# Optimization experiments

Hardware: AMD Instinct MI355X
Metric: run time of the kernel (lower is better)

## Reference

```python
import jax, jax.numpy as jnp
import numpy as np

B, N, C, H, W = 4, 8, 256, 64, 64
SCALE = 2
D = C * SCALE  # embed_dim*scale, head_size with n_heads=1
EPS = 1e-6


def setup_inputs() -> dict:
    key = jax.random.key(0)
    ks = jax.random.split(key, 6)
    sc = lambda k, sh, f: jax.random.normal(k, sh, jnp.float32) * f
    return {
        "q": jax.random.normal(ks[0], (B, C), jnp.float32),
        "c": jax.random.normal(ks[1], (B, N, C, H, W), jnp.float32),
        "g": jnp.ones((C,), jnp.float32),                 # RMSNorm weight
        "Wq": sc(ks[2], (D, C), C ** -0.5),               # proj_q weight
        "Wkv": sc(ks[3], (2 * D, C), C ** -0.5),          # proj_kv weight
        "Wo": sc(ks[4], (C, D), D ** -0.5),               # proj_out weight
        "bo": jnp.zeros((C,), jnp.float32),               # proj_out bias
    }


def reference(q, c, g, Wq, Wkv, Wo, bo):
    # c: [B,N,C,H,W] -> [B,H,W,N,C]
    cp = jnp.transpose(c, (0, 3, 4, 1, 2))
    # RMSNorm over channel dim
    cn = cp * jax.lax.rsqrt(jnp.mean(cp * cp, axis=-1, keepdims=True) + EPS) * g
    # per-pixel, per-token k/v projection: [B,H,W,N,2D]
    kv = jnp.einsum('bhwnc,dc->bhwnd', cn, Wkv)
    k, v = jnp.split(kv, 2, axis=-1)                      # each [B,H,W,N,D]
    qp = q @ Wq.T                                         # [B,D]
    # broadcast single query over spatial grid; softmax over N context tokens
    dots = jnp.einsum('bd,bhwnd->bhwn', qp, k) * (D ** -0.5)
    att = jax.nn.softmax(dots, axis=-1)                   # [B,H,W,N]
    hvec = jnp.einsum('bhwn,bhwnd->bhwd', att, v)         # [B,H,W,D]
    out = hvec @ Wo.T + bo                                # [B,H,W,C]
    return jnp.transpose(out, (0, 3, 1, 2))               # [B,C,H,W]
```

## Files before the change

### kernel.cpp

```cpp
#include <hip/hip_runtime.h>


typedef __attribute__((ext_vector_type(8))) short short8;
typedef __attribute__((ext_vector_type(4))) float floatx4;

static __device__ __forceinline__ short f2bf(float f) {
  unsigned u = __float_as_uint(f);
  u += 0x7fffu + ((u >> 16) & 1u);
  return (short)(u >> 16);
}

__global__ __launch_bounds__(256) void pre_kernel(
    const float* __restrict__ q, const float* __restrict__ g,
    const float* __restrict__ Wq, const float* __restrict__ Wkv,
    const float* __restrict__ Wo, unsigned char* __restrict__ ws) {
  short* WovgB = (short*)ws;
  float* gqk = (float*)(ws + 131072);
  const int blk = blockIdx.x, tid = threadIdx.x;
  if (blk < 256) {
    const int i = blk, c = tid;
    float s = 0.f;
    #pragma unroll 16
    for (int d = 0; d < 512; ++d)
      s = fmaf(Wo[i * 512 + d], Wkv[(512 + d) * 256 + c], s);
    const int it = i >> 4, m = i & 15;
    const int sg = c >> 5, q2 = (c >> 3) & 3, jj = c & 7;
    WovgB[((((it * 8 + sg) * 4 + q2) * 16) + m) * 8 + jj] = f2bf(s * g[c]);
  } else {
    const int b = blk - 256;
    __shared__ float qps[512];
    for (int d = tid; d < 512; d += 256) {
      float s = 0.f;
      #pragma unroll 16
      for (int cc = 0; cc < 256; ++cc)
        s = fmaf(Wq[d * 256 + cc], q[b * 256 + cc], s);
      qps[d] = s;
    }
    __syncthreads();
    const int c = tid;
    float s = 0.f;
    #pragma unroll 16
    for (int d = 0; d < 512; ++d)
      s = fmaf(Wkv[d * 256 + c], qps[d], s);
    gqk[b * 256 + c] = s * g[c] * 0.044194173824159216f;
  }
}

__global__ __launch_bounds__(256, 2) void attn_kernel(
    const float* __restrict__ cin, const float* __restrict__ bo,
    const unsigned char* __restrict__ ws, float* __restrict__ out) {
  const short8* Av = (const short8*)ws;
  const float* gqk = (const float*)(ws + 131072);
  const int blk = blockIdx.x;
  const int b = blk >> 7, h = (blk >> 1) & 63, hf = blk & 1;
  const int tid = threadIdx.x;
  const int lane = tid & 63, w = tid >> 6;
  const int px = lane & 31, cgh = lane >> 5;
  const int cg = w * 2 + cgh;

  __shared__ short tB[8][2][64][8];
  __shared__ float redS[2][4][32], redD[2][4][32];

  float rg[32];
  #pragma unroll
  for (int j = 0; j < 32; ++j) rg[j] = gqk[b * 256 + cg * 32 + j];

  float t_reg[32];
  #pragma unroll
  for (int j = 0; j < 32; ++j) t_reg[j] = 0.f;
  float mM = -1e30f, zZ = 0.f;

  const float* cb = cin + ((size_t)(b * 8) * 256 + cg * 32) * 4096
                        + h * 64 + hf * 32 + px;
  for (int n = 0; n < 8; ++n) {
    const float* cp = cb + (size_t)n * 256 * 4096;
    float vals[32];
    #pragma unroll
    for (int j = 0; j < 32; ++j) vals[j] = cp[(size_t)j * 4096];
    float ssq = 0.f, dt = 0.f;
    #pragma unroll
    for (int j = 0; j < 32; ++j) {
      ssq = fmaf(vals[j], vals[j], ssq);
      dt = fmaf(vals[j], rg[j], dt);
    }
    ssq += __shfl_xor(ssq, 32);
    dt  += __shfl_xor(dt, 32);
    if (cgh == 0) { redS[n & 1][w][px] = ssq; redD[n & 1][w][px] = dt; }
    __syncthreads();
    float S = 0.f, Dt = 0.f;
    #pragma unroll
    for (int ww = 0; ww < 4; ++ww) { S += redS[n & 1][ww][px]; Dt += redD[n & 1][ww][px]; }
    const float invr = rsqrtf(S * (1.f / 256.f) + 1e-6f);
    const float d = Dt * invr;
    const float mn = fmaxf(mM, d);
    const float al = __expf(mM - mn);
    const float e = __expf(d - mn);
    zZ = zZ * al + e;
    mM = mn;
    const float wn = e * invr;
    #pragma unroll
    for (int j = 0; j < 32; ++j) t_reg[j] = fmaf(wn, vals[j], t_reg[j] * al);
  }

  {
    const float invZ = 1.f / zZ;
    const int nt = px >> 4, mm = px & 15;
    #pragma unroll
    for (int qq = 0; qq < 4; ++qq) {
      short8 pk;
      #pragma unroll
      for (int jj = 0; jj < 8; ++jj) pk[jj] = f2bf(t_reg[qq * 8 + jj] * invZ);
      *(short8*)(&tB[cg][nt][qq * 16 + mm][0]) = pk;
    }
  }
  __syncthreads();

  const int ig = __builtin_amdgcn_readfirstlane(w);
  const int q = lane >> 4, m = lane & 15;
  const short8* Bv = (const short8*)tB;
  floatx4 acc[4][2];
  #pragma unroll
  for (int mt = 0; mt < 4; ++mt)
    #pragma unroll
    for (int nt = 0; nt < 2; ++nt) acc[mt][nt] = (floatx4){0.f, 0.f, 0.f, 0.f};
  #pragma unroll
  for (int s = 0; s < 8; ++s) {
    short8 a[4];
    #pragma unroll
    for (int mt = 0; mt < 4; ++mt)
      a[mt] = Av[(((ig * 4 + mt) * 8 + s) * 4 + q) * 16 + m];
    #pragma unroll
    for (int nt = 0; nt < 2; ++nt) {
      const short8 bf = Bv[(s * 2 + nt) * 64 + lane];
      #pragma unroll
      for (int mt = 0; mt < 4; ++mt)
        acc[mt][nt] = __builtin_amdgcn_mfma_f32_16x16x32_bf16(a[mt], bf, acc[mt][nt], 0, 0, 0);
    }
  }
  float* ob = out + (size_t)b * 256 * 4096 + h * 64 + hf * 32;
  #pragma unroll
  for (int mt = 0; mt < 4; ++mt) {
    float bov[4];
    #pragma unroll
    for (int r = 0; r < 4; ++r) bov[r] = bo[ig * 64 + mt * 16 + q * 4 + r];
    #pragma unroll
    for (int nt = 0; nt < 2; ++nt)
      #pragma unroll
      for (int r = 0; r < 4; ++r) {
        const int i = ig * 64 + mt * 16 + q * 4 + r;
        ob[(size_t)i * 4096 + nt * 16 + m] = acc[mt][nt][r] + bov[r];
      }
  }
}

extern "C" void kernel_launch(void* const* d_in, const int* in_sizes, int n_in,
                              void* d_out, int out_size, void* d_ws, size_t ws_size,
                              hipStream_t stream) {
  const float* q   = (const float*)d_in[0];
  const float* c   = (const float*)d_in[1];
  const float* g   = (const float*)d_in[2];
  const float* Wq  = (const float*)d_in[3];
  const float* Wkv = (const float*)d_in[4];
  const float* Wo  = (const float*)d_in[5];
  const float* bo  = (const float*)d_in[6];
  float* out = (float*)d_out;
  unsigned char* ws = (unsigned char*)d_ws;
  pre_kernel<<<260, 256, 0, stream>>>(q, g, Wq, Wkv, Wo, ws);
  attn_kernel<<<512, 256, 0, stream>>>(c, bo, ws, out);
}
```

Baseline: 249.4 us.

## Double attention block to 512 threads and batch Wo·Wv precompute rows

The attention kernel now uses 512 threads per block. Each thread handles 16 channels instead of 32, which halves per-thread register use and the serial load chain. The output projection is split across 8 waves, each covering 32 output rows. The precompute kernel now computes 4 output rows per block, reusing each Wkv load across the 4 rows, so it launches 68 blocks instead of 260. The trade-offs are a wider cross-wave reduction on every iteration and fewer blocks for the weight precompute.

```diff
diff --git a/kernel.cpp b/kernel.cpp
--- a/kernel.cpp
+++ b/kernel.cpp
@@ -17,17 +17,28 @@
   short* WovgB = (short*)ws;
   float* gqk = (float*)(ws + 131072);
   const int blk = blockIdx.x, tid = threadIdx.x;
-  if (blk < 256) {
-    const int i = blk, c = tid;
-    float s = 0.f;
-    #pragma unroll 16
-    for (int d = 0; d < 512; ++d)
-      s = fmaf(Wo[i * 512 + d], Wkv[(512 + d) * 256 + c], s);
-    const int it = i >> 4, m = i & 15;
+  if (blk < 64) {
+    const int c = tid, i0 = blk * 4;
+    float s0 = 0.f, s1 = 0.f, s2 = 0.f, s3 = 0.f;
+    #pragma unroll 8
+    for (int d = 0; d < 512; ++d) {
+      const float wv = Wkv[(512 + d) * 256 + c];
+      s0 = fmaf(Wo[(i0 + 0) * 512 + d], wv, s0);
+      s1 = fmaf(Wo[(i0 + 1) * 512 + d], wv, s1);
+      s2 = fmaf(Wo[(i0 + 2) * 512 + d], wv, s2);
+      s3 = fmaf(Wo[(i0 + 3) * 512 + d], wv, s3);
+    }
+    const float gc = g[c];
+    const float sv[4] = {s0, s1, s2, s3};
     const int sg = c >> 5, q2 = (c >> 3) & 3, jj = c & 7;
-    WovgB[((((it * 8 + sg) * 4 + q2) * 16) + m) * 8 + jj] = f2bf(s * g[c]);
+    #pragma unroll
+    for (int r = 0; r < 4; ++r) {
+      const int i = i0 + r;
+      const int it = i >> 4, m = i & 15;
+      WovgB[((((it * 8 + sg) * 4 + q2) * 16) + m) * 8 + jj] = f2bf(sv[r] * gc);
+    }
   } else {
-    const int b = blk - 256;
+    const int b = blk - 64;
     __shared__ float qps[512];
     for (int d = tid; d < 512; d += 256) {
       float s = 0.f;
@@ -46,7 +57,7 @@
   }
 }
 
-__global__ __launch_bounds__(256, 2) void attn_kernel(
+__global__ __launch_bounds__(512, 4) void attn_kernel(
     const float* __restrict__ cin, const float* __restrict__ bo,
     const unsigned char* __restrict__ ws, float* __restrict__ out) {
   const short8* Av = (const short8*)ws;
@@ -59,27 +70,27 @@
   const int cg = w * 2 + cgh;
 
   __shared__ short tB[8][2][64][8];
-  __shared__ float redS[2][4][32], redD[2][4][32];
+  __shared__ float redS[2][8][32], redD[2][8][32];
 
-  float rg[32];
+  float rg[16];
   #pragma unroll
-  for (int j = 0; j < 32; ++j) rg[j] = gqk[b * 256 + cg * 32 + j];
+  for (int j = 0; j < 16; ++j) rg[j] = gqk[b * 256 + cg * 16 + j];
 
-  float t_reg[32];
+  float t_reg[16];
   #pragma unroll
-  for (int j = 0; j < 32; ++j) t_reg[j] = 0.f;
+  for (int j = 0; j < 16; ++j) t_reg[j] = 0.f;
   float mM = -1e30f, zZ = 0.f;
 
-  const float* cb = cin + ((size_t)(b * 8) * 256 + cg * 32) * 4096
+  const float* cb = cin + ((size_t)(b * 8) * 256 + cg * 16) * 4096
                         + h * 64 + hf * 32 + px;
   for (int n = 0; n < 8; ++n) {
     const float* cp = cb + (size_t)n * 256 * 4096;
-    float vals[32];
+    float vals[16];
     #pragma unroll
-    for (int j = 0; j < 32; ++j) vals[j] = cp[(size_t)j * 4096];
+    for (int j = 0; j < 16; ++j) vals[j] = cp[(size_t)j * 4096];
     float ssq = 0.f, dt = 0.f;
     #pragma unroll
-    for (int j = 0; j < 32; ++j) {
+    for (int j = 0; j < 16; ++j) {
       ssq = fmaf(vals[j], vals[j], ssq);
       dt = fmaf(vals[j], rg[j], dt);
     }
@@ -89,7 +100,7 @@
     __syncthreads();
     float S = 0.f, Dt = 0.f;
     #pragma unroll
-    for (int ww = 0; ww < 4; ++ww) { S += redS[n & 1][ww][px]; Dt += redD[n & 1][ww][px]; }
+    for (int ww = 0; ww < 8; ++ww) { S += redS[n & 1][ww][px]; Dt += redD[n & 1][ww][px]; }
     const float invr = rsqrtf(S * (1.f / 256.f) + 1e-6f);
     const float d = Dt * invr;
     const float mn = fmaxf(mM, d);
@@ -99,55 +110,56 @@
     mM = mn;
     const float wn = e * invr;
     #pragma unroll
-    for (int j = 0; j < 32; ++j) t_reg[j] = fmaf(wn, vals[j], t_reg[j] * al);
+    for (int j = 0; j < 16; ++j) t_reg[j] = fmaf(wn, vals[j], t_reg[j] * al);
   }
 
   {
     const float invZ = 1.f / zZ;
     const int nt = px >> 4, mm = px & 15;
+    const int s = cg >> 1;
     #pragma unroll
-    for (int qq = 0; qq < 4; ++qq) {
+    for (int h2 = 0; h2 < 2; ++h2) {
+      const int q = (cg & 1) * 2 + h2;
       short8 pk;
       #pragma unroll
-      for (int jj = 0; jj < 8; ++jj) pk[jj] = f2bf(t_reg[qq * 8 + jj] * invZ);
-      *(short8*)(&tB[cg][nt][qq * 16 + mm][0]) = pk;
+      for (int jj = 0; jj < 8; ++jj) pk[jj] = f2bf(t_reg[h2 * 8 + jj] * invZ);
+      *(short8*)(&tB[s][nt][q * 16 + mm][0]) = pk;
     }
   }
   __syncthreads();
 
-  const int ig = __builtin_amdgcn_readfirstlane(w);
   const int q = lane >> 4, m = lane & 15;
   const short8* Bv = (const short8*)tB;
-  floatx4 acc[4][2];
+  floatx4 acc[2][2];
   #pragma unroll
-  for (int mt = 0; mt < 4; ++mt)
+  for (int mt = 0; mt < 2; ++mt)
     #pragma unroll
     for (int nt = 0; nt < 2; ++nt) acc[mt][nt] = (floatx4){0.f, 0.f, 0.f, 0.f};
   #pragma unroll
   for (int s = 0; s < 8; ++s) {
-    short8 a[4];
+    short8 a[2];
     #pragma unroll
-    for (int mt = 0; mt < 4; ++mt)
-      a[mt] = Av[(((ig * 4 + mt) * 8 + s) * 4 + q) * 16 + m];
+    for (int mt = 0; mt < 2; ++mt)
+      a[mt] = Av[(((w * 2 + mt) * 8 + s) * 4 + q) * 16 + m];
     #pragma unroll
     for (int nt = 0; nt < 2; ++nt) {
       const short8 bf = Bv[(s * 2 + nt) * 64 + lane];
       #pragma unroll
-      for (int mt = 0; mt < 4; ++mt)
+      for (int mt = 0; mt < 2; ++mt)
         acc[mt][nt] = __builtin_amdgcn_mfma_f32_16x16x32_bf16(a[mt], bf, acc[mt][nt], 0, 0, 0);
     }
   }
   float* ob = out + (size_t)b * 256 * 4096 + h * 64 + hf * 32;
   #pragma unroll
-  for (int mt = 0; mt < 4; ++mt) {
+  for (int mt = 0; mt < 2; ++mt) {
     float bov[4];
     #pragma unroll
-    for (int r = 0; r < 4; ++r) bov[r] = bo[ig * 64 + mt * 16 + q * 4 + r];
+    for (int r = 0; r < 4; ++r) bov[r] = bo[w * 32 + mt * 16 + q * 4 + r];
     #pragma unroll
     for (int nt = 0; nt < 2; ++nt)
       #pragma unroll
       for (int r = 0; r < 4; ++r) {
-        const int i = ig * 64 + mt * 16 + q * 4 + r;
+        const int i = w * 32 + mt * 16 + q * 4 + r;
         ob[(size_t)i * 4096 + nt * 16 + m] = acc[mt][nt][r] + bov[r];
       }
   }
@@ -165,6 +177,6 @@
   const float* bo  = (const float*)d_in[6];
   float* out = (float*)d_out;
   unsigned char* ws = (unsigned char*)d_ws;
-  pre_kernel<<<260, 256, 0, stream>>>(q, g, Wq, Wkv, Wo, ws);
-  attn_kernel<<<512, 256, 0, stream>>>(c, bo, ws, out);
+  pre_kernel<<<68, 256, 0, stream>>>(q, g, Wq, Wkv, Wo, ws);
+  attn_kernel<<<512, 512, 0, stream>>>(c, bo, ws, out);
 }
```

Result: slower. 312.8 us (+25.4%).
